# Optimization experiments

Hardware: AMD Instinct MI355X
Metric: run time of the kernel (lower is better)

Reference implementation:

```python
import jax, jax.numpy as jnp
from jax import lax
import numpy as np

IN, G, H, L = 128, 5, 512, 256   # input_size, n_genres, hidden_dim, latent_dim
E = 2 * H                         # encoder_hidden_dim (bidirectional)
B, T = 128, 256
SLOPE = 0.01                      # torch LeakyReLU default


def _gru(xt, h, Wih, Whh, bih, bhh):
    # torch.nn.GRUCell: gates ordered r, z, n
    gi = xt @ Wih.T + bih         # [B, 3H]
    gh = h @ Whh.T + bhh          # [B, 3H]
    ir, iz, inn = jnp.split(gi, 3, axis=-1)
    hr, hz, hn = jnp.split(gh, 3, axis=-1)
    r = jax.nn.sigmoid(ir + hr)
    z = jax.nn.sigmoid(iz + hz)
    n = jnp.tanh(inn + r * hn)
    return (1.0 - z) * n + z * h


def _leaky(v):
    return jnp.where(v >= 0, v, SLOPE * v)


def setup_inputs() -> dict:
    key = jax.random.key(0)
    ks = jax.random.split(key, 32)
    it = iter(range(32))

    def p(shape, fan_in):
        s = 1.0 / np.sqrt(fan_in)
        return jax.random.uniform(ks[next(it)], shape, jnp.float32, -s, s)

    inp = {
        "x": jax.random.normal(ks[next(it)], (B, T, IN + G), jnp.float32),
        "latent_genre_vec": jax.random.uniform(ks[next(it)], (B, G), jnp.float32),
        "eps": jax.random.normal(ks[next(it)], (B, L - G), jnp.float32),
    }
    # forward encoder GRUCell (input IN+G -> H)
    inp["Wih_e"] = p((3 * H, IN + G), H); inp["Whh_e"] = p((3 * H, H), H)
    inp["bih_e"] = p((3 * H,), H);        inp["bhh_e"] = p((3 * H,), H)
    # backward encoder GRUCell
    inp["Wih_be"] = p((3 * H, IN + G), H); inp["Whh_be"] = p((3 * H, H), H)
    inp["bih_be"] = p((3 * H,), H);        inp["bhh_be"] = p((3 * H,), H)
    # decoder GRUCell (input IN -> H)
    inp["Wih_d"] = p((3 * H, IN), H); inp["Whh_d"] = p((3 * H, H), H)
    inp["bih_d"] = p((3 * H,), H);    inp["bhh_d"] = p((3 * H,), H)
    # fc_mu: [Linear(E,E)+LeakyReLU, Linear(E, L-G)]
    inp["W_mu0"] = p((E, E), E); inp["b_mu0"] = p((E,), E)
    inp["W_mu1"] = p((L - G, E), E); inp["b_mu1"] = p((L - G,), E)
    # fc_logvar
    inp["W_lv0"] = p((E, E), E); inp["b_lv0"] = p((E,), E)
    inp["W_lv1"] = p((L - G, E), E); inp["b_lv1"] = p((L - G,), E)
    # fc_latent: [Linear(L,L)+LeakyReLU, Linear(L, H)]
    inp["W_lat0"] = p((L, L), L); inp["b_lat0"] = p((L,), L)
    inp["W_lat1"] = p((H, L), L); inp["b_lat1"] = p((H,), L)
    # fc_decoder final Linear(H, IN) (fc_decoder[0] is dead code in the original loop)
    inp["W_dec1"] = p((IN, H), H); inp["b_dec1"] = p((IN,), H)
    return inp


def reference(x, latent_genre_vec, eps,
              Wih_e, Whh_e, bih_e, bhh_e,
              Wih_be, Whh_be, bih_be, bhh_be,
              Wih_d, Whh_d, bih_d, bhh_d,
              W_mu0, b_mu0, W_mu1, b_mu1,
              W_lv0, b_lv0, W_lv1, b_lv1,
              W_lat0, b_lat0, W_lat1, b_lat1,
              W_dec1, b_dec1):
    b = x.shape[0]
    xs = jnp.swapaxes(x, 0, 1)  # [T, B, IN+G]
    h0 = jnp.zeros((b, H), x.dtype)

    def enc_step(h, xt):
        return _gru(xt, h, Wih_e, Whh_e, bih_e, bhh_e), None

    def benc_step(h, xt):
        return _gru(xt, h, Wih_be, Whh_be, bih_be, bhh_be), None

    h_fwd, _ = lax.scan(enc_step, h0, xs)
    h_bwd, _ = lax.scan(benc_step, h0, xs, reverse=True)
    hidden = jnp.concatenate([h_fwd, h_bwd], axis=1)  # [B, 2H]

    mu = _leaky(hidden @ W_mu0.T + b_mu0) @ W_mu1.T + b_mu1        # [B, L-G]
    logvar = _leaky(hidden @ W_lv0.T + b_lv0) @ W_lv1.T + b_lv1    # [B, L-G]

    z = mu + jnp.exp(0.5 * logvar) * eps
    z = jnp.concatenate([z, latent_genre_vec], axis=1)             # [B, L]

    dec_h = _leaky(z @ W_lat0.T + b_lat0) @ W_lat1.T + b_lat1      # [B, H]

    note0 = x[:, 0, :IN]  # [B, IN]

    def dec_step(carry, _):
        h, note = carry
        h = _gru(note, h, Wih_d, Whh_d, bih_d, bhh_d)
        # faithful to original: final fc_decoder layer applied to hidden
        note = h @ W_dec1.T + b_dec1
        return (h, note), note

    _, notes = lax.scan(dec_step, (dec_h, note0), None, length=x.shape[1] - 1)
    output = jnp.concatenate([note0[:, None, :], jnp.swapaxes(notes, 0, 1)], axis=1)  # [B, T, IN]
    return output, mu, logvar
```

## Files before the change

### kernel.cpp

```cpp
#include <hip/hip_runtime.h>

#define B_ 128
#define T_ 256
#define IN_ 128
#define G_ 5
#define H_ 512
#define G3_ 1536
#define E_ 1024
#define L_ 256
#define LG_ 251
#define INPG_ 133

#define MU_OFF (B_*T_*IN_)
#define LV_OFF (MU_OFF + B_*LG_)

#define ERS 684
#define DRS 524

typedef __attribute__((ext_vector_type(8))) short bf16x8;
typedef __attribute__((ext_vector_type(4))) float f32x4;
typedef unsigned long long u64;

__device__ __forceinline__ float bf2f(unsigned short s) {
    return __uint_as_float(((unsigned)s) << 16);
}
__device__ __forceinline__ unsigned short f2bf(float f) {
    unsigned x = __float_as_uint(f);
    unsigned r = (x + 0x7fffu + ((x >> 16) & 1u)) >> 16;
    return (unsigned short)r;
}
__device__ __forceinline__ float sigf(float v) {
    return __builtin_amdgcn_rcpf(1.f + __expf(-v));
}
__device__ __forceinline__ float ftanh(float x) {
    x = fminf(15.f, fmaxf(-15.f, x));
    float e = __expf(2.f * x);
    return (e - 1.f) * __builtin_amdgcn_rcpf(e + 1.f);
}
__device__ __forceinline__ u64 ld_h64(const void* p) {
    return __hip_atomic_load((const u64*)p, __ATOMIC_RELAXED, __HIP_MEMORY_SCOPE_AGENT);
}
__device__ __forceinline__ void st_h32(void* p, unsigned v) {
    __hip_atomic_store((unsigned*)p, v, __ATOMIC_RELAXED, __HIP_MEMORY_SCOPE_AGENT);
}
__device__ __forceinline__ u64 badm(u64 v) {
    u64 x = ~v;
    return (x - 0x0001000100010001ull) & ~x & 0x8000800080008000ull;
}
__device__ __forceinline__ bf16x8 mk_frag(u64 lo, u64 hi) {
    bf16x8 a;
    ((u64*)&a)[0] = lo; ((u64*)&a)[1] = hi;
    return a;
}
__device__ __forceinline__ bf16x8 lds_frag(const ushort* p) {
    u64 lo = *(const u64*)p;
    u64 hi = *(const u64*)(p + 4);
    return mk_frag(lo, hi);
}


__global__ void xpad_k(const float* __restrict__ x, ushort* __restrict__ xb) {
    int id = blockIdx.x * 256 + threadIdx.x;
    if (id >= T_ * B_ * 160) return;
    int t = id / (B_ * 160);
    int rem = id - t * (B_ * 160);
    int b = rem / 160, c = rem - b * 160;
    float v = (c < INPG_) ? x[((size_t)b * T_ + t) * INPG_ + c] : 0.f;
    xb[id] = f2bf(v);
}

__global__ void pack_we(const float* __restrict__ Wih_f, const float* __restrict__ Whh_f,
                        const float* __restrict__ Wih_b, const float* __restrict__ Whh_b,
                        ushort* __restrict__ WE) {
    int id = blockIdx.x * 256 + threadIdx.x;
    int lane = id & 63;
    int rest = id >> 6;
    int ks = rest % 63;
    int cb = (rest / 63) & 31;
    int dir = rest / (63 * 32);
    if (dir >= 2) return;
    const float* Wih = dir ? Wih_b : Wih_f;
    const float* Whh = dir ? Whh_b : Whh_f;
    int n = lane & 15, kb = lane >> 4;
    int p, ksp;
    if (ks < 21)      { p = 0; ksp = ks; }
    else if (ks < 42) { p = 1; ksp = ks - 21; }
    else if (ks < 47) { p = 2; ksp = ks - 42; }
    else              { p = 3; ksp = ks - 47; }
    int j = cb * 16 + n;
    int row = (p == 0) ? j : (p == 1) ? 512 + j : 1024 + j;
    #pragma unroll
    for (int e = 0; e < 8; ++e) {
        int k = ksp * 32 + kb * 8 + e;
        float v;
        if (p == 3)      v = Whh[(size_t)row * 512 + k];
        else if (p == 2) v = (k < INPG_) ? Wih[(size_t)row * INPG_ + k] : 0.f;
        else v = (k < INPG_) ? Wih[(size_t)row * INPG_ + k]
               : (k < 160)   ? 0.f
               : Whh[(size_t)row * 512 + (k - 160)];
        WE[(size_t)id * 8 + e] = f2bf(v);
    }
}

__global__ void wfused_k(const float* __restrict__ Wih_d, const float* __restrict__ Wdec1,
                         float* __restrict__ Wf) {
    int id = blockIdx.x * 256 + threadIdx.x;
    if (id >= G3_ * H_) return;
    int r = id >> 9, c = id & 511;
    float s = 0.f;
    for (int m = 0; m < 128; ++m)
        s += Wih_d[(size_t)r * 128 + m] * Wdec1[(size_t)m * 512 + c];
    Wf[id] = s;
}

__global__ void bfi_k(const float* __restrict__ Wih_d, const float* __restrict__ b_dec1,
                      const float* __restrict__ bih_d, float* __restrict__ bfi) {
    int r = blockIdx.x * 256 + threadIdx.x;
    if (r >= G3_) return;
    float s = bih_d[r];
    for (int m = 0; m < 128; ++m)
        s += Wih_d[(size_t)r * 128 + m] * b_dec1[m];
    bfi[r] = s;
}

__global__ void pack_wd(const float* __restrict__ Wf, const float* __restrict__ Whh,
                        ushort* __restrict__ WD, int fused) {
    int id = blockIdx.x * 256 + threadIdx.x;
    int lane = id & 63;
    int rest = id >> 6;
    int ks = rest & 63;
    int cb = rest >> 6;
    if (cb >= 32) return;
    int p = ks >> 4, ksp = ks & 15;
    int n = lane & 15, kb = lane >> 4;
    int j = cb * 16 + n;
    int row = (p == 0) ? j : (p == 1) ? 512 + j : 1024 + j;
    #pragma unroll
    for (int e = 0; e < 8; ++e) {
        int k = ksp * 32 + kb * 8 + e;
        float v;
        if (p <= 1) v = fused ? (Wf[(size_t)row * 512 + k] + Whh[(size_t)row * 512 + k])
                              : Whh[(size_t)row * 512 + k];
        else if (p == 2) v = fused ? Wf[(size_t)row * 512 + k] : 0.f;
        else v = Whh[(size_t)row * 512 + k];
        WD[(size_t)id * 8 + e] = f2bf(v);
    }
}

__global__ void pack_wdec(const float* __restrict__ Wdec1, ushort* __restrict__ pk) {
    int id = blockIdx.x * 256 + threadIdx.x;
    if (id >= 8192) return;
    int lane = id & 63, ch = id >> 6;
    int nt = ch >> 4, ks = ch & 15;
    int n = nt * 16 + (lane & 15);
    int k0 = ks * 32 + (lane >> 4) * 8;
    #pragma unroll
    for (int e = 0; e < 8; ++e)
        pk[(size_t)id * 8 + e] = f2bf(Wdec1[(size_t)n * 512 + k0 + e]);
}

__global__ void poison_k(ulonglong2* __restrict__ hb, ulonglong2* __restrict__ hist) {
    size_t id = (size_t)blockIdx.x * 256 + threadIdx.x;
    ulonglong2 p; p.x = ~0ull; p.y = ~0ull;
    if (id < (size_t)256 * 2 * 65536 / 8) hb[id] = p;
    if (id < (size_t)255 * 65536 / 8)     hist[id] = p;
}

__global__ void note0_k2(const float* __restrict__ x, float* __restrict__ out,
                         float* __restrict__ note0f) {
    int id = blockIdx.x * 256 + threadIdx.x;
    if (id >= B_ * IN_) return;
    int b = id >> 7, n = id & 127;
    float v = x[((size_t)b * T_) * INPG_ + n];
    out[((size_t)b * T_) * IN_ + n] = v;
    note0f[(size_t)b * 128 + n] = v;
}

__global__ void cvt_h0(const float* __restrict__ src, ushort* __restrict__ dst) {
    int id = blockIdx.x * 256 + threadIdx.x;
    if (id < B_ * H_) dst[id] = f2bf(src[id]);
}

__global__ void tile_w(const float* __restrict__ W, ushort4* __restrict__ out,
                       int N, int K, int KC) {
    int id = blockIdx.x * 256 + threadIdx.x;
    if (id >= KC * N) return;
    int kc = id / N, n = id - kc * N;
    int k = kc * 4;
    ushort4 u;
    u.x = f2bf(k + 0 < K ? W[(size_t)n * K + k + 0] : 0.f);
    u.y = f2bf(k + 1 < K ? W[(size_t)n * K + k + 1] : 0.f);
    u.z = f2bf(k + 2 < K ? W[(size_t)n * K + k + 2] : 0.f);
    u.w = f2bf(k + 3 < K ? W[(size_t)n * K + k + 3] : 0.f);
    out[(size_t)kc * N + n] = u;
}

#define MFMA16(a, b, c) __builtin_amdgcn_mfma_f32_16x16x32_bf16((a), (b), (c), 0, 0, 0)

__global__ __launch_bounds__(256) void enc_persist(
    const ushort* __restrict__ xb16, const ushort* __restrict__ WE,
    ushort* __restrict__ hb,
    float* __restrict__ hidden,
    const float* __restrict__ bih_f, const float* __restrict__ bhh_f,
    const float* __restrict__ bih_b, const float* __restrict__ bhh_b)
{
    __shared__ ushort As[32 * ERS];
    __shared__ ushort Ws[63 * 512];
    __shared__ float gs[4][512];
    int bid = blockIdx.x;
    int dir = bid >> 7, bt = (bid >> 5) & 3, cb = bid & 31;
    int b0 = bt * 32;
    int tid = threadIdx.x;
    const float* bih = dir ? bih_b : bih_f;
    const float* bhh = dir ? bhh_b : bhh_f;

    {
        const ushort* src = WE + (size_t)((dir * 32 + cb) * 63) * 512;
        for (int c = tid; c < 4032; c += 256)
            *(uint4*)&Ws[c * 8] = *(const uint4*)&src[c * 8];
    }
    for (int i = 0; i < 16; ++i) {
        int c = tid + i * 256;
        int row = c >> 7, off = c & 127;
        *(u64*)((char*)As + row * (ERS * 2) + 320 + off * 8) = 0ull;
    }
    {
        const ushort* xr = xb16 + (size_t)(dir ? 255 : 0) * (B_ * 160);
        for (int i = 0; i < 3; ++i) {
            int c = tid + i * 256;
            if (c < 640) {
                int row = c / 20, off = c - row * 20;
                ulonglong2 v = *(const ulonglong2*)(xr + (size_t)(b0 + row) * 160 + off * 8);
                char* d = (char*)As + row * (ERS * 2) + off * 16;
                *(u64*)d = v.x; *(u64*)(d + 8) = v.y;
            }
        }
    }
    int bA = tid >> 3;
    int j0 = cb * 16 + 2 * (tid & 7), j1 = j0 + 1;
    float b_r0 = bih[j0] + bhh[j0],             b_r1 = bih[j1] + bhh[j1];
    float b_z0 = bih[512 + j0] + bhh[512 + j0], b_z1 = bih[512 + j1] + bhh[512 + j1];
    float b_in0 = bih[1024 + j0],               b_in1 = bih[1024 + j1];
    float b_hn0 = bhh[1024 + j0],               b_hn1 = bhh[1024 + j1];
    float hc0 = 0.f, hc1 = 0.f;

    int lane = tid & 63, wv = tid >> 6;
    int m = lane & 15, kb = lane >> 4;
    int nk  = (wv == 2) ? 5 : (wv == 3) ? 16 : 21;
    int ksb = (wv == 0) ? 0 : (wv == 1) ? 21 : (wv == 2) ? 42 : 47;
    int kcol0 = (wv == 3) ? 160 : 0;
    int ai0 = m * ERS + kcol0 + kb * 8;
    int ai1 = (16 + m) * ERS + kcol0 + kb * 8;

    for (int t = 0; t < T_; ++t) {
        ushort* hout = hb + ((size_t)t * 2 + dir) * 65536;
        if (t > 0) {
            const ushort* hin = hb + ((size_t)(t - 1) * 2 + dir) * 65536;
            u64 vb[16];
            for (;;) {
                #pragma unroll
                for (int i = 0; i < 16; ++i) {
                    int c = tid + i * 256;
                    int row = c >> 7, off = c & 127;
                    vb[i] = ld_h64(hin + (size_t)(b0 + row) * 512 + off * 4);
                }
                u64 bad = 0;
                #pragma unroll
                for (int i = 0; i < 16; ++i) bad |= badm(vb[i]);
                if (__all(bad == 0)) break;
            }
            #pragma unroll
            for (int i = 0; i < 16; ++i) {
                int c = tid + i * 256;
                int row = c >> 7, off = c & 127;
                *(u64*)((char*)As + row * (ERS * 2) + 320 + off * 8) = vb[i];
            }
        }
        __syncthreads();
        f32x4 acc0 = {0.f,0.f,0.f,0.f}, acc1 = {0.f,0.f,0.f,0.f};
        const ushort* Bp = &Ws[ksb * 512 + lane * 8];
        for (int ks = 0; ks < nk; ++ks) {
            bf16x8 bfr = *(const bf16x8*)(Bp + (size_t)ks * 512);
            bf16x8 a0 = lds_frag(&As[ai0 + ks * 32]);
            bf16x8 a1 = lds_frag(&As[ai1 + ks * 32]);
            acc0 = MFMA16(a0, bfr, acc0);
            acc1 = MFMA16(a1, bfr, acc1);
        }
        #pragma unroll
        for (int i = 0; i < 4; ++i) {
            gs[wv][(kb * 4 + i) * 16 + m] = acc0[i];
            gs[wv][(16 + kb * 4 + i) * 16 + m] = acc1[i];
        }
        __syncthreads();
        {
            int o0 = 2 * tid, o1 = o0 + 1;
            float r0 = sigf(gs[0][o0] + b_r0);
            float z0 = sigf(gs[1][o0] + b_z0);
            float n0 = ftanh(gs[2][o0] + b_in0 + r0 * (gs[3][o0] + b_hn0));
            hc0 = (1.f - z0) * n0 + z0 * hc0;
            float r1 = sigf(gs[0][o1] + b_r1);
            float z1 = sigf(gs[1][o1] + b_z1);
            float n1 = ftanh(gs[2][o1] + b_in1 + r1 * (gs[3][o1] + b_hn1));
            hc1 = (1.f - z1) * n1 + z1 * hc1;
            unsigned pkd = (unsigned)f2bf(hc0) | ((unsigned)f2bf(hc1) << 16);
            st_h32((char*)hout + ((size_t)(b0 + bA) * 512 + j0) * 2, pkd);
        }
        if (t == 255) {
            float2 hv = {hc0, hc1};
            *(float2*)&hidden[(size_t)(b0 + bA) * 1024 + dir * 512 + j0] = hv;
        } else {
            int tt2 = dir ? (254 - t) : (t + 1);
            const ushort* xr2 = xb16 + (size_t)tt2 * (B_ * 160);
            for (int i2 = 0; i2 < 3; ++i2) {
                int c = tid + i2 * 256;
                if (c < 640) {
                    int row = c / 20, off2 = c - row * 20;
                    ulonglong2 v = *(const ulonglong2*)(xr2 + (size_t)(b0 + row) * 160 + off2 * 8);
                    char* d = (char*)As + row * (ERS * 2) + off2 * 16;
                    *(u64*)d = v.x; *(u64*)(d + 8) = v.y;
                }
            }
        }
    }
}

__global__ __launch_bounds__(64, 1) void dec_step1(
    const ushort* __restrict__ hdec0, const ushort* __restrict__ WD1,
    const float* __restrict__ h0f, const float* __restrict__ gi0,
    const float* __restrict__ bhh, ushort* __restrict__ hist0,
    float* __restrict__ h1f)
{
    int bid = blockIdx.x;
    int rt = bid >> 5, cb = bid & 31;
    int lane = threadIdx.x;
    int m = lane & 15, kb = lane >> 4;
    int arow = rt * 16 + m;
    int j = cb * 16 + m;
    int orow = rt * 16 + kb * 4;
    const ushort* hr = hdec0 + (size_t)arow * 512 + kb * 8;
    bf16x8 af[16];
    #pragma unroll
    for (int ks = 0; ks < 16; ++ks)
        af[ks] = *(const bf16x8*)(hr + ks * 32);
    const ushort* w1 = WD1 + (size_t)(cb * 64) * 512 + lane * 8;
    f32x4 aR = {0.f,0.f,0.f,0.f}, aZ = {0.f,0.f,0.f,0.f}, aGh = {0.f,0.f,0.f,0.f};
    #pragma unroll
    for (int ks = 0; ks < 16; ++ks) {
        aR = MFMA16(af[ks], *(const bf16x8*)(w1 + (size_t)ks * 512), aR);
        aZ = MFMA16(af[ks], *(const bf16x8*)(w1 + (size_t)(16 + ks) * 512), aZ);
        aGh = MFMA16(af[ks], *(const bf16x8*)(w1 + (size_t)(48 + ks) * 512), aGh);
    }
    float bh_r = bhh[j], bh_z = bhh[512 + j], bh_n = bhh[1024 + j];
    #pragma unroll
    for (int i = 0; i < 4; ++i) {
        int rg = orow + i;
        float gr = gi0[(size_t)rg * G3_ + j];
        float gz = gi0[(size_t)rg * G3_ + 512 + j];
        float gn = gi0[(size_t)rg * G3_ + 1024 + j];
        float h0 = h0f[(size_t)rg * 512 + j];
        float r = sigf(aR[i] + gr + bh_r);
        float z = sigf(aZ[i] + gz + bh_z);
        float n = ftanh(gn + r * (aGh[i] + bh_n));
        float h1 = (1.f - z) * n + z * h0;
        h1f[(size_t)rg * 512 + j] = h1;
        hist0[(size_t)rg * 512 + j] = f2bf(h1);
    }
}

__global__ __launch_bounds__(256) void dec_persist(
    const ushort* __restrict__ WD2, ushort* __restrict__ hist,
    const float* __restrict__ h1f, const float* __restrict__ bfi,
    const float* __restrict__ bhh)
{
    __shared__ ushort As[32 * DRS];
    __shared__ ushort Ws[64 * 512];
    __shared__ float gs[4][512];
    int bid = blockIdx.x;
    int bt = bid >> 5, cb = bid & 31;
    int b0 = bt * 32, tid = threadIdx.x;
    {
        const ushort* src = WD2 + (size_t)(cb * 64) * 512;
        for (int c = tid; c < 4096; c += 256)
            *(uint4*)&Ws[c * 8] = *(const uint4*)&src[c * 8];
    }
    int bA = tid >> 3;
    int j0 = cb * 16 + 2 * (tid & 7), j1 = j0 + 1;
    float f_r0 = bfi[j0] + bhh[j0],             f_r1 = bfi[j1] + bhh[j1];
    float f_z0 = bfi[512 + j0] + bhh[512 + j0], f_z1 = bfi[512 + j1] + bhh[512 + j1];
    float f_in0 = bfi[1024 + j0],               f_in1 = bfi[1024 + j1];
    float f_hn0 = bhh[1024 + j0],               f_hn1 = bhh[1024 + j1];
    float hc0 = h1f[(size_t)(b0 + bA) * 512 + j0];
    float hc1 = h1f[(size_t)(b0 + bA) * 512 + j1];

    int lane = tid & 63, wv = tid >> 6;
    int m = lane & 15, kb = lane >> 4;
    int ai0 = m * DRS + kb * 8, ai1 = (16 + m) * DRS + kb * 8;

    for (int t = 2; t < T_; ++t) {
        const ushort* hin = hist + (size_t)(t - 2) * 65536;
        u64 vb[16];
        for (;;) {
            #pragma unroll
            for (int i = 0; i < 16; ++i) {
                int c = tid + i * 256;
                int row = c >> 7, off = c & 127;
                vb[i] = ld_h64(hin + (size_t)(b0 + row) * 512 + off * 4);
            }
            u64 bad = 0;
            #pragma unroll
            for (int i = 0; i < 16; ++i) bad |= badm(vb[i]);
            if (__all(bad == 0)) break;
        }
        #pragma unroll
        for (int i = 0; i < 16; ++i) {
            int c = tid + i * 256;
            int row = c >> 7, off = c & 127;
            *(u64*)((char*)As + row * (DRS * 2) + off * 8) = vb[i];
        }
        __syncthreads();
        f32x4 acc0 = {0.f,0.f,0.f,0.f}, acc1 = {0.f,0.f,0.f,0.f};
        const ushort* Bp = &Ws[(wv * 16) * 512 + lane * 8];
        for (int ks = 0; ks < 16; ++ks) {
            bf16x8 bfr = *(const bf16x8*)(Bp + (size_t)ks * 512);
            bf16x8 a0 = lds_frag(&As[ai0 + ks * 32]);
            bf16x8 a1 = lds_frag(&As[ai1 + ks * 32]);
            acc0 = MFMA16(a0, bfr, acc0);
            acc1 = MFMA16(a1, bfr, acc1);
        }
        #pragma unroll
        for (int i = 0; i < 4; ++i) {
            gs[wv][(kb * 4 + i) * 16 + m] = acc0[i];
            gs[wv][(16 + kb * 4 + i) * 16 + m] = acc1[i];
        }
        __syncthreads();
        {
            int o0 = 2 * tid, o1 = o0 + 1;
            float r0 = sigf(gs[0][o0] + f_r0);
            float z0 = sigf(gs[1][o0] + f_z0);
            float n0 = ftanh(gs[2][o0] + f_in0 + r0 * (gs[3][o0] + f_hn0));
            hc0 = (1.f - z0) * n0 + z0 * hc0;
            float r1 = sigf(gs[0][o1] + f_r1);
            float z1 = sigf(gs[1][o1] + f_z1);
            float n1 = ftanh(gs[2][o1] + f_in1 + r1 * (gs[3][o1] + f_hn1));
            hc1 = (1.f - z1) * n1 + z1 * hc1;
            unsigned pkd = (unsigned)f2bf(hc0) | ((unsigned)f2bf(hc1) << 16);
            st_h32((char*)(hist + (size_t)(t - 1) * 65536) +
                   ((size_t)(b0 + bA) * 512 + j0) * 2, pkd);
        }
    }
}

__global__ __launch_bounds__(256) void notes_mfma(
    const ushort* __restrict__ hist, const ushort* __restrict__ pk,
    const float* __restrict__ bd, float* __restrict__ out)
{
    __shared__ ushort hs[32 * DRS];
    int m0 = blockIdx.x * 32;
    int tid = threadIdx.x;
    #pragma unroll
    for (int i = 0; i < 8; ++i) {
        int c = tid + i * 256;
        int row = c >> 6, off = c & 63;
        ulonglong2 v = *(const ulonglong2*)(hist + (size_t)(m0 + row) * 512 + off * 8);
        char* d = (char*)hs + row * (DRS * 2) + off * 16;
        *(u64*)d = v.x; *(u64*)(d + 8) = v.y;
    }
    __syncthreads();
    int lane = tid & 63, wv = tid >> 6;
    int m = lane & 15, kb = lane >> 4;
    int nt0 = wv * 2;
    f32x4 acc00 = {0.f,0.f,0.f,0.f}, acc01 = {0.f,0.f,0.f,0.f};
    f32x4 acc10 = {0.f,0.f,0.f,0.f}, acc11 = {0.f,0.f,0.f,0.f};
    for (int ks = 0; ks < 16; ++ks) {
        bf16x8 a0 = lds_frag(&hs[m * DRS + ks * 32 + kb * 8]);
        bf16x8 a1 = lds_frag(&hs[(16 + m) * DRS + ks * 32 + kb * 8]);
        bf16x8 bf0 = *(const bf16x8*)&pk[(size_t)((nt0 * 16 + ks) * 64 + lane) * 8];
        bf16x8 bf1 = *(const bf16x8*)&pk[(size_t)(((nt0 + 1) * 16 + ks) * 64 + lane) * 8];
        acc00 = MFMA16(a0, bf0, acc00);
        acc01 = MFMA16(a0, bf1, acc01);
        acc10 = MFMA16(a1, bf0, acc10);
        acc11 = MFMA16(a1, bf1, acc11);
    }
    int n0 = nt0 * 16 + (lane & 15), n1 = (nt0 + 1) * 16 + (lane & 15);
    #pragma unroll
    for (int i = 0; i < 4; ++i) {
        int r0 = m0 + kb * 4 + i;
        int r1 = r0 + 16;
        int t0 = r0 >> 7, b0r = r0 & 127;
        int t1 = r1 >> 7, b1r = r1 & 127;
        out[((size_t)b0r * T_ + (t0 + 1)) * IN_ + n0] = acc00[i] + bd[n0];
        out[((size_t)b0r * T_ + (t0 + 1)) * IN_ + n1] = acc01[i] + bd[n1];
        out[((size_t)b1r * T_ + (t1 + 1)) * IN_ + n0] = acc10[i] + bd[n0];
        out[((size_t)b1r * T_ + (t1 + 1)) * IN_ + n1] = acc11[i] + bd[n1];
    }
}

__global__ __launch_bounds__(256) void gemm_t4(
    const float* __restrict__ A, const ushort4* __restrict__ Wt,
    const float* __restrict__ bias, float* __restrict__ C,
    int M, int N, int K, int act)
{
    int nb = blockIdx.x, mb = blockIdx.y;
    int tid = threadIdx.x;
    int n = nb * 64 + (tid & 63);
    int mq = tid >> 6;
    int m0 = mb * 32;
    __shared__ float Asm[32][36];
    float acc[8];
    #pragma unroll
    for (int i = 0; i < 8; ++i) acc[i] = 0.f;
    for (int k0 = 0; k0 < K; k0 += 32) {
        int r = tid >> 3, c = (tid & 7) << 2;
        float4 v = *(const float4*)&A[(size_t)(m0 + r) * K + k0 + c];
        Asm[r][c] = v.x; Asm[r][c+1] = v.y; Asm[r][c+2] = v.z; Asm[r][c+3] = v.w;
        __syncthreads();
        #pragma unroll
        for (int kc = 0; kc < 8; ++kc) {
            float w0 = 0.f, w1 = 0.f, w2 = 0.f, w3 = 0.f;
            if (n < N) {
                ushort4 u = Wt[(size_t)((k0 >> 2) + kc) * N + n];
                w0 = bf2f(u.x); w1 = bf2f(u.y); w2 = bf2f(u.z); w3 = bf2f(u.w);
            }
            #pragma unroll
            for (int i = 0; i < 8; ++i) {
                int mm = mq * 8 + i;
                acc[i] += Asm[mm][kc*4+0]*w0 + Asm[mm][kc*4+1]*w1
                        + Asm[mm][kc*4+2]*w2 + Asm[mm][kc*4+3]*w3;
            }
        }
        __syncthreads();
    }
    if (n < N) {
        #pragma unroll
        for (int i = 0; i < 8; ++i) {
            int mm = m0 + mq * 8 + i;
            float v = acc[i] + bias[n];
            if (act == 1) v = (v >= 0.f) ? v : 0.01f * v;
            C[(size_t)mm * N + n] = v;
        }
    }
}

__global__ void z_k(const float* __restrict__ out, const float* __restrict__ eps,
                    const float* __restrict__ genre, float* __restrict__ zc) {
    int id = blockIdx.x * 256 + threadIdx.x;
    if (id >= B_ * L_) return;
    int b = id >> 8, c = id & 255;
    float v;
    if (c < LG_) {
        float mu = out[MU_OFF + (size_t)b * LG_ + c];
        float lv = out[LV_OFF + (size_t)b * LG_ + c];
        v = mu + expf(0.5f * lv) * eps[(size_t)b * LG_ + c];
    } else {
        v = genre[(size_t)b * G_ + (c - LG_)];
    }
    zc[id] = v;
}

extern "C" void kernel_launch(void* const* d_in, const int* in_sizes, int n_in,
                              void* d_out, int out_size, void* d_ws, size_t ws_size,
                              hipStream_t stream) {
    (void)in_sizes; (void)n_in; (void)out_size; (void)ws_size;
    const float* x      = (const float*)d_in[0];
    const float* genre  = (const float*)d_in[1];
    const float* eps    = (const float*)d_in[2];
    const float* Wih_e  = (const float*)d_in[3];
    const float* Whh_e  = (const float*)d_in[4];
    const float* bih_e  = (const float*)d_in[5];
    const float* bhh_e  = (const float*)d_in[6];
    const float* Wih_be = (const float*)d_in[7];
    const float* Whh_be = (const float*)d_in[8];
    const float* bih_be = (const float*)d_in[9];
    const float* bhh_be = (const float*)d_in[10];
    const float* Wih_d  = (const float*)d_in[11];
    const float* Whh_d  = (const float*)d_in[12];
    const float* bih_d  = (const float*)d_in[13];
    const float* bhh_d  = (const float*)d_in[14];
    const float* W_mu0  = (const float*)d_in[15];
    const float* b_mu0  = (const float*)d_in[16];
    const float* W_mu1  = (const float*)d_in[17];
    const float* b_mu1  = (const float*)d_in[18];
    const float* W_lv0  = (const float*)d_in[19];
    const float* b_lv0  = (const float*)d_in[20];
    const float* W_lv1  = (const float*)d_in[21];
    const float* b_lv1  = (const float*)d_in[22];
    const float* W_lat0 = (const float*)d_in[23];
    const float* b_lat0 = (const float*)d_in[24];
    const float* W_lat1 = (const float*)d_in[25];
    const float* b_lat1 = (const float*)d_in[26];
    const float* W_dec1 = (const float*)d_in[27];
    const float* b_dec1 = (const float*)d_in[28];
    float* out = (float*)d_out;

    char* ws = (char*)d_ws;
    size_t off = 0;
    auto alloc = [&](size_t bytes) -> char* {
        char* p = ws + off;
        off = (off + bytes + 255) & ~(size_t)255;
        return p;
    };
    ushort* xb16  = (ushort*)alloc((size_t)T_ * B_ * 160 * 2);
    ushort* WE    = (ushort*)alloc((size_t)2 * 32 * 63 * 512 * 2);
    ushort* WD2   = (ushort*)alloc((size_t)32 * 64 * 512 * 2);
    ushort* WD1   = (ushort*)alloc((size_t)32 * 64 * 512 * 2);
    float*  Wf    = (float*)alloc((size_t)G3_ * H_ * 4);
    float*  bfi   = (float*)alloc(G3_ * 4);
    ushort* hb_e  = (ushort*)alloc((size_t)256 * 2 * 65536 * 2);
    ushort* hist  = (ushort*)alloc((size_t)255 * 65536 * 2);
    ushort* hdec0 = (ushort*)alloc((size_t)65536 * 2);
    ushort* pkdec = (ushort*)alloc((size_t)8192 * 8 * 2);
    float*  note0f= (float*)alloc((size_t)B_ * 128 * 4);
    float*  gi0   = (float*)alloc((size_t)B_ * G3_ * 4);
    float*  hidden= (float*)alloc((size_t)B_ * E_ * 4);
    float*  t0buf = (float*)alloc((size_t)B_ * E_ * 4);
    float*  t1buf = (float*)alloc((size_t)B_ * E_ * 4);
    float*  zcbuf = (float*)alloc((size_t)B_ * L_ * 4);
    float*  t2buf = (float*)alloc((size_t)B_ * L_ * 4);
    float*  t3buf = (float*)alloc((size_t)B_ * H_ * 4);
    float*  h1f   = (float*)alloc((size_t)B_ * H_ * 4);

    ushort4* T_Wmu0  = (ushort4*)alloc((size_t)256 * E_ * 8);
    ushort4* T_Wmu1  = (ushort4*)alloc((size_t)256 * LG_ * 8);
    ushort4* T_Wlv0  = (ushort4*)alloc((size_t)256 * E_ * 8);
    ushort4* T_Wlv1  = (ushort4*)alloc((size_t)256 * LG_ * 8);
    ushort4* T_Wlat0 = (ushort4*)alloc((size_t)64 * L_ * 8);
    ushort4* T_Wlat1 = (ushort4*)alloc((size_t)64 * H_ * 8);
    ushort4* T_Wihd  = (ushort4*)alloc((size_t)32 * G3_ * 8);

    xpad_k<<<(T_ * B_ * 160 + 255) / 256, 256, 0, stream>>>(x, xb16);
    pack_we<<<1008, 256, 0, stream>>>(Wih_e, Whh_e, Wih_be, Whh_be, WE);
    wfused_k<<<(G3_ * H_ + 255) / 256, 256, 0, stream>>>(Wih_d, W_dec1, Wf);
    bfi_k<<<6, 256, 0, stream>>>(Wih_d, b_dec1, bih_d, bfi);
    pack_wd<<<512, 256, 0, stream>>>(Wf, Whh_d, WD2, 1);
    pack_wd<<<512, 256, 0, stream>>>(Wf, Whh_d, WD1, 0);
    pack_wdec<<<32, 256, 0, stream>>>(W_dec1, pkdec);
    poison_k<<<16384, 256, 0, stream>>>((ulonglong2*)hb_e, (ulonglong2*)hist);
    note0_k2<<<(B_ * IN_ + 255) / 256, 256, 0, stream>>>(x, out, note0f);

    auto tile = [&](const float* W, ushort4* dst, int N, int K) {
        int KC = (K + 3) / 4;
        tile_w<<<(KC * N + 255) / 256, 256, 0, stream>>>(W, dst, N, K, KC);
    };
    tile(W_mu0,  T_Wmu0,  E_,  E_);
    tile(W_mu1,  T_Wmu1,  LG_, E_);
    tile(W_lv0,  T_Wlv0,  E_,  E_);
    tile(W_lv1,  T_Wlv1,  LG_, E_);
    tile(W_lat0, T_Wlat0, L_,  L_);
    tile(W_lat1, T_Wlat1, H_,  L_);
    tile(Wih_d,  T_Wihd,  G3_, IN_);

    enc_persist<<<256, 256, 0, stream>>>(xb16, WE, hb_e, hidden,
                                         bih_e, bhh_e, bih_be, bhh_be);

    {
        dim3 g1(16, 4), g2(4, 4), g3(4, 4), g4(8, 4), g5(24, 4);
        gemm_t4<<<g1, 256, 0, stream>>>(hidden, T_Wmu0, b_mu0, t0buf, B_, E_, E_, 1);
        gemm_t4<<<g2, 256, 0, stream>>>(t0buf, T_Wmu1, b_mu1, out + MU_OFF, B_, LG_, E_, 0);
        gemm_t4<<<g1, 256, 0, stream>>>(hidden, T_Wlv0, b_lv0, t1buf, B_, E_, E_, 1);
        gemm_t4<<<g2, 256, 0, stream>>>(t1buf, T_Wlv1, b_lv1, out + LV_OFF, B_, LG_, E_, 0);
        z_k<<<(B_ * L_ + 255) / 256, 256, 0, stream>>>(out, eps, genre, zcbuf);
        gemm_t4<<<g3, 256, 0, stream>>>(zcbuf, T_Wlat0, b_lat0, t2buf, B_, L_, L_, 1);
        gemm_t4<<<g4, 256, 0, stream>>>(t2buf, T_Wlat1, b_lat1, t3buf, B_, H_, L_, 0);
        gemm_t4<<<g5, 256, 0, stream>>>(note0f, T_Wihd, bih_d, gi0, B_, G3_, IN_, 0);
    }
    cvt_h0<<<(B_ * H_ + 255) / 256, 256, 0, stream>>>(t3buf, hdec0);

    dec_step1<<<256, 64, 0, stream>>>(hdec0, WD1, t3buf, gi0, bhh_d, hist, h1f);
    dec_persist<<<128, 256, 0, stream>>>(WD2, hist, h1f, bfi, bhh_d);

    notes_mfma<<<1020, 256, 0, stream>>>(hist, pkdec, b_dec1, out);
}
```

Before: 2.253 ms.

## Overlap input-projection MFMAs with hidden-state polling in encoder GRU loop

Splits each wave's K-loop into an x-part (5 k-steps, input columns already staged in LDS) and an h-part (16 k-steps). The global loads of the previous hidden state are issued first, the x-part MFMAs run while those loads are in flight, and only then is the readiness poll checked and h written to LDS. This aims to hide cross-block synchronisation latency on the recurrent critical path. It adds an extra __syncthreads per step (and one before the loop) to protect the LDS x-tile reuse, which adds barrier cost.

```diff
diff --git a/kernel.cpp b/kernel.cpp
--- a/kernel.cpp
+++ b/kernel.cpp
@@ -246,28 +246,49 @@
 
     int lane = tid & 63, wv = tid >> 6;
     int m = lane & 15, kb = lane >> 4;
-    int nk  = (wv == 2) ? 5 : (wv == 3) ? 16 : 21;
-    int ksb = (wv == 0) ? 0 : (wv == 1) ? 21 : (wv == 2) ? 42 : 47;
-    int kcol0 = (wv == 3) ? 160 : 0;
-    int ai0 = m * ERS + kcol0 + kb * 8;
-    int ai1 = (16 + m) * ERS + kcol0 + kb * 8;
+    int xB = (wv == 0) ? 0 : (wv == 1) ? 21 : 42;
+    int hB = (wv == 0) ? 5 : (wv == 1) ? 26 : 47;
+    int axi0 = m * ERS + kb * 8;
+    int axi1 = (16 + m) * ERS + kb * 8;
+    int ahi0 = m * ERS + 160 + kb * 8;
+    int ahi1 = (16 + m) * ERS + 160 + kb * 8;
+
+    __syncthreads();
 
     for (int t = 0; t < T_; ++t) {
         ushort* hout = hb + ((size_t)t * 2 + dir) * 65536;
+        const ushort* hin = hb + ((size_t)(t - 1) * 2 + dir) * 65536;
+        u64 vb[16];
         if (t > 0) {
-            const ushort* hin = hb + ((size_t)(t - 1) * 2 + dir) * 65536;
-            u64 vb[16];
+            #pragma unroll
+            for (int i = 0; i < 16; ++i) {
+                int c = tid + i * 256;
+                int row = c >> 7, off = c & 127;
+                vb[i] = ld_h64(hin + (size_t)(b0 + row) * 512 + off * 4);
+            }
+        }
+        f32x4 acc0 = {0.f,0.f,0.f,0.f}, acc1 = {0.f,0.f,0.f,0.f};
+        if (wv != 3) {
+            const ushort* Bx = &Ws[xB * 512 + lane * 8];
+            #pragma unroll
+            for (int ks = 0; ks < 5; ++ks) {
+                bf16x8 bfr = *(const bf16x8*)(Bx + (size_t)ks * 512);
+                acc0 = MFMA16(lds_frag(&As[axi0 + ks * 32]), bfr, acc0);
+                acc1 = MFMA16(lds_frag(&As[axi1 + ks * 32]), bfr, acc1);
+            }
+        }
+        if (t > 0) {
             for (;;) {
+                u64 bad = 0;
+                #pragma unroll
+                for (int i = 0; i < 16; ++i) bad |= badm(vb[i]);
+                if (__all(bad == 0)) break;
                 #pragma unroll
                 for (int i = 0; i < 16; ++i) {
                     int c = tid + i * 256;
                     int row = c >> 7, off = c & 127;
                     vb[i] = ld_h64(hin + (size_t)(b0 + row) * 512 + off * 4);
                 }
-                u64 bad = 0;
-                #pragma unroll
-                for (int i = 0; i < 16; ++i) bad |= badm(vb[i]);
-                if (__all(bad == 0)) break;
             }
             #pragma unroll
             for (int i = 0; i < 16; ++i) {
@@ -277,14 +298,13 @@
             }
         }
         __syncthreads();
-        f32x4 acc0 = {0.f,0.f,0.f,0.f}, acc1 = {0.f,0.f,0.f,0.f};
-        const ushort* Bp = &Ws[ksb * 512 + lane * 8];
-        for (int ks = 0; ks < nk; ++ks) {
-            bf16x8 bfr = *(const bf16x8*)(Bp + (size_t)ks * 512);
-            bf16x8 a0 = lds_frag(&As[ai0 + ks * 32]);
-            bf16x8 a1 = lds_frag(&As[ai1 + ks * 32]);
-            acc0 = MFMA16(a0, bfr, acc0);
-            acc1 = MFMA16(a1, bfr, acc1);
+        if (wv != 2) {
+            const ushort* Bh = &Ws[hB * 512 + lane * 8];
+            for (int ks = 0; ks < 16; ++ks) {
+                bf16x8 bfr = *(const bf16x8*)(Bh + (size_t)ks * 512);
+                acc0 = MFMA16(lds_frag(&As[ahi0 + ks * 32]), bfr, acc0);
+                acc1 = MFMA16(lds_frag(&As[ahi1 + ks * 32]), bfr, acc1);
+            }
         }
         #pragma unroll
         for (int i = 0; i < 4; ++i) {
@@ -321,6 +341,7 @@
                 }
             }
         }
+        __syncthreads();
     }
 }
 
```

Measured after the change: 2.198 ms (median of 2 runs). 2.4% less time.
